# Kernel tuning notes

Hardware: AMD Instinct MI355X
Metric: run time of the kernel (lower is better)

## Reference

```python
import jax, jax.numpy as jnp
import numpy as np

MD = 4            # max_displacement
DP = 1            # dilation_patch
PATCH = 2 * MD + 1  # 9
# kernel_size=1, stride=1, padding=0, dilation=1 -> oH=H, oW=W


def setup_inputs() -> dict:
    key = jax.random.key(0)
    k1, k2 = jax.random.split(key)
    N, C, H, W = 8, 256, 128, 128
    input1 = jax.random.normal(k1, (N, C, H, W), dtype=jnp.float32)
    input2 = jax.random.normal(k2, (N, C, H, W), dtype=jnp.float32)
    return {"input1": input1, "input2": input2}


def _correlation(input1, input2):
    # out[n, py, px, y, x] = sum_c input1[n,c,y,x] * input2[n,c, y+(py-MD)*DP, x+(px-MD)*DP]
    # with zero padding for out-of-bounds input2 positions (mmcv semantics, no
    # normalization by channel count).
    N, C, H, W = input1.shape
    pad = MD * DP
    x2 = jnp.pad(input2, ((0, 0), (0, 0), (pad, pad), (pad, pad)))
    rows = []
    for py in range(PATCH):  # small fixed displacement grid (9x9)
        cols = []
        for px in range(PATCH):
            sh, sw = py * DP, px * DP
            x2s = x2[:, :, sh:sh + H, sw:sw + W]  # shifted input2, [N,C,H,W]
            cols.append(jnp.einsum('nchw,nchw->nhw', input1, x2s))
        rows.append(jnp.stack(cols, axis=1))  # [N, PATCH, H, W]
    return jnp.stack(rows, axis=1)  # [N, PATCH, PATCH, H, W]


def reference(input1, input2):
    return _correlation(input1, input2)
```

## Files before the change

### kernel.cpp

```cpp
#include <hip/hip_runtime.h>
#include <limits.h>

typedef __attribute__((ext_vector_type(8))) short short8v;
typedef __attribute__((ext_vector_type(4))) float f32x4;

#define H_  128
#define W_  128
#define C_  256
#define HW_ 16384

#define MFMA32(a, b, c) __builtin_amdgcn_mfma_f32_16x16x32_bf16(a, b, c, 0, 0, 0)

__device__ __forceinline__ short bf16b(float f) {
    unsigned u = __float_as_uint(f);
    u += 0x7fffu + ((u >> 16) & 1u);
    return (short)(u >> 16);
}
__device__ __forceinline__ unsigned bf16pk(float lo, float hi) {
    unsigned ul = __float_as_uint(lo);
    ul += 0x7fffu + ((ul >> 16) & 1u);
    unsigned uh = __float_as_uint(hi);
    uh += 0x7fffu + ((uh >> 16) & 1u);
    return (ul >> 16) | (uh & 0xffff0000u);
}

__global__ __launch_bounds__(512, 2)
void corr_kernel(const float* __restrict__ in1, const float* __restrict__ in2,
                 float* __restrict__ out)
{
    __shared__ __attribute__((aligned(16))) unsigned char smem[3 * 49152];
    short*    lds  = (short*)smem;
    unsigned* ldsI = (unsigned*)smem;
    float*    ldso = (float*)smem;

    const int tid  = threadIdx.x;
    const int lane = tid & 63;
    const int wid  = tid >> 6;
    const int m    = lane & 15;
    const int g    = lane >> 4;

    int bid = blockIdx.x;
    int swz = (bid & 7) * 64 + (bid >> 3);
    int n   = swz >> 6;
    int h0  = ((swz >> 3) & 7) << 4;
    int w0  = (swz & 7) << 4;

    const float* in1n = in1 + (size_t)n * (C_ * HW_);
    const float* in2n = in2 + (size_t)n * (C_ * HW_);

    int lwdw[5]; int gof0[5];
#pragma unroll
    for (int s = 0; s < 5; ++s) {
        int u    = tid + s * 512;
        bool act = (u < 2304);
        int q    = u % 6;
        int rest = u / 6;
        int kp   = rest & 15;
        int r    = rest >> 4;
        int row  = h0 - 4 + r;
        int col0 = w0 - 4 + 4 * q;
        bool inb = act && ((unsigned)row < 128u) && ((unsigned)col0 < 125u);
        int  cc  = 8 * (kp >> 2) + 2 * (kp & 3);
        gof0[s]  = inb ? (cc * HW_ + row * W_ + col0) : INT_MIN;
        lwdw[s]  = ((r * 4 + (kp >> 2)) * 32 + 4 * q) * 4 + (kp & 3);
    }
    const int abase = (8 * g) * HW_ + (h0 + 2 * wid) * W_ + (w0 + m);

    {
        short8v z = (short8v)0;
        short8v* zp = (short8v*)lds;
#pragma unroll
        for (int i = 0; i < 18; ++i) zp[tid + i * 512] = z;
    }

    f32x4 acc[2][9][2];
#pragma unroll
    for (int a = 0; a < 2; ++a)
#pragma unroll
        for (int d = 0; d < 9; ++d)
#pragma unroll
            for (int t = 0; t < 2; ++t)
                acc[a][d][t] = (f32x4){0.f, 0.f, 0.f, 0.f};

    __syncthreads();
    __builtin_amdgcn_sched_barrier(0);

    f32x4 sf[5][2];
    float afn[2][8];

#pragma unroll
    for (int s = 0; s < 5; ++s)
#pragma unroll
        for (int e = 0; e < 2; ++e) {
            f32x4 v = (f32x4){0.f, 0.f, 0.f, 0.f};
            if (gof0[s] != INT_MIN) v = *(const f32x4*)(in2n + gof0[s] + e * HW_);
            sf[s][e] = v;
        }
#pragma unroll
    for (int s = 0; s < 5; ++s)
        if (tid + s * 512 < 2304) {
#pragma unroll
            for (int d = 0; d < 4; ++d)
                ldsI[lwdw[s] + 4 * d] = bf16pk(sf[s][0][d], sf[s][1][d]);
        }
#pragma unroll
    for (int s = 0; s < 5; ++s)
#pragma unroll
        for (int e = 0; e < 2; ++e) {
            f32x4 v = (f32x4){0.f, 0.f, 0.f, 0.f};
            if (gof0[s] != INT_MIN) v = *(const f32x4*)(in2n + gof0[s] + e * HW_ + 32 * HW_);
            sf[s][e] = v;
        }
#pragma unroll
    for (int rs = 0; rs < 2; ++rs)
#pragma unroll
        for (int i = 0; i < 8; ++i)
            afn[rs][i] = in1n[abase + i * HW_ + rs * W_];

#pragma unroll 1
    for (int t = 0; t < 8; ++t) {
        __syncthreads();
        __builtin_amdgcn_sched_barrier(0);
        const int bcur  = t % 3;
        const int wnext = (t + 1) % 3;

        short8v a8[2];
#pragma unroll
        for (int rs = 0; rs < 2; ++rs)
#pragma unroll
            for (int i = 0; i < 8; ++i) a8[rs][i] = bf16b(afn[rs][i]);

        if (t < 7) {
            unsigned* wp = ldsI + wnext * 12288;
#pragma unroll
            for (int s = 0; s < 5; ++s)
                if (tid + s * 512 < 2304) {
#pragma unroll
                    for (int d = 0; d < 4; ++d)
                        wp[lwdw[s] + 4 * d] = bf16pk(sf[s][0][d], sf[s][1][d]);
                }
        }
        if (t < 6) {
            const int koff = (t + 2) * 32 * HW_;
#pragma unroll
            for (int s = 0; s < 5; ++s)
#pragma unroll
                for (int e = 0; e < 2; ++e) {
                    f32x4 v = (f32x4){0.f, 0.f, 0.f, 0.f};
                    if (gof0[s] != INT_MIN) v = *(const f32x4*)(in2n + gof0[s] + e * HW_ + koff);
                    sf[s][e] = v;
                }
        }
        if (t < 7) {
            const int akoff = (t + 1) * 32 * HW_;
#pragma unroll
            for (int rs = 0; rs < 2; ++rs)
#pragma unroll
                for (int i = 0; i < 8; ++i)
                    afn[rs][i] = in1n[abase + (akoff + i * HW_) + rs * W_];
        }

        const short* lb = lds + bcur * 24576;
#pragma unroll
        for (int rr = 0; rr < 10; ++rr) {
            int ro = (((2 * wid + rr) * 4 + g) * 32) * 8;
            short8v b0 = *(const short8v*)&lb[ro + m * 8];
            short8v b1 = *(const short8v*)&lb[ro + (16 + m) * 8];
            if (rr <= 8) {
                acc[0][rr][0] = MFMA32(a8[0], b0, acc[0][rr][0]);
                acc[0][rr][1] = MFMA32(a8[0], b1, acc[0][rr][1]);
            }
            if (rr >= 1) {
                acc[1][rr - 1][0] = MFMA32(a8[1], b0, acc[1][rr - 1][0]);
                acc[1][rr - 1][1] = MFMA32(a8[1], b1, acc[1][rr - 1][1]);
            }
        }
    }

    const size_t outb = (size_t)n * 81 * HW_;
#pragma unroll
    for (int dy = 0; dy < 9; ++dy) {
        __syncthreads();
        __builtin_amdgcn_sched_barrier(0);
#pragma unroll
        for (int rs = 0; rs < 2; ++rs) {
            int hl = 2 * wid + rs;
#pragma unroll
            for (int nt = 0; nt < 2; ++nt) {
#pragma unroll
                for (int i = 0; i < 4; ++i) {
                    int mm = 4 * g + i;
                    int dx = nt * 16 + m - mm;
                    if (dx >= 0 && dx < 9)
                        ldso[dx * 257 + hl * 16 + mm] = acc[rs][dy][nt][i];
                }
            }
        }
        __syncthreads();
        __builtin_amdgcn_sched_barrier(0);
#pragma unroll
        for (int e = 0; e < 5; ++e) {
            int t = tid + e * 512;
            if (t < 2304) {
                int dx  = t >> 8;
                int rem = t & 255;
                out[outb + (size_t)(dy * 9 + dx) * HW_ +
                    (size_t)(h0 + (rem >> 4)) * W_ + (w0 + (rem & 15))] = ldso[dx * 257 + rem];
            }
        }
    }
}

extern "C" void kernel_launch(void* const* d_in, const int* in_sizes, int n_in,
                              void* d_out, int out_size, void* d_ws, size_t ws_size,
                              hipStream_t stream) {
    const float* in1 = (const float*)d_in[0];
    const float* in2 = (const float*)d_in[1];
    float* out = (float*)d_out;
    corr_kernel<<<dim3(512), dim3(512), 0, stream>>>(in1, in2, out);
}
```

Measured before the change: 98.24 us.

## Use 1024-thread blocks with single LDS buffer, swizzled layout, and one-shot epilogue

Doubles the threads per block to 1024 so each wave owns a single output row instead of two, halving per-thread accumulators and register pressure. The triple-buffered LDS staging is replaced by a single buffer with two barriers per K step, using a rotated (XOR-like) dword layout to avoid bank conflicts instead of zero-initialised padding. The epilogue stages all 81 displacement planes in LDS at once and writes them out in a single pass instead of nine barrier-separated passes. This trades software pipelining depth for more waves and fewer per-thread registers, and may expose global load latency more.

```diff
diff --git a/kernel.cpp b/kernel.cpp
--- a/kernel.cpp
+++ b/kernel.cpp
@@ -4,9 +4,7 @@
 typedef __attribute__((ext_vector_type(8))) short short8v;
 typedef __attribute__((ext_vector_type(4))) float f32x4;
 
-#define H_  128
 #define W_  128
-#define C_  256
 #define HW_ 16384
 
 #define MFMA32(a, b, c) __builtin_amdgcn_mfma_f32_16x16x32_bf16(a, b, c, 0, 0, 0)
@@ -24,11 +22,11 @@
     return (ul >> 16) | (uh & 0xffff0000u);
 }
 
-__global__ __launch_bounds__(512, 2)
+__global__ __launch_bounds__(1024)
 void corr_kernel(const float* __restrict__ in1, const float* __restrict__ in2,
                  float* __restrict__ out)
 {
-    __shared__ __attribute__((aligned(16))) unsigned char smem[3 * 49152];
+    __shared__ __attribute__((aligned(16))) unsigned char smem[84992];
     short*    lds  = (short*)smem;
     unsigned* ldsI = (unsigned*)smem;
     float*    ldso = (float*)smem;
@@ -45,51 +43,41 @@
     int h0  = ((swz >> 3) & 7) << 4;
     int w0  = (swz & 7) << 4;
 
-    const float* in1n = in1 + (size_t)n * (C_ * HW_);
-    const float* in2n = in2 + (size_t)n * (C_ * HW_);
+    const float* in1n = in1 + (size_t)n * (256 * HW_);
+    const float* in2n = in2 + (size_t)n * (256 * HW_);
 
-    int lwdw[5]; int gof0[5];
+    int gof0[3], wbas[3], wrot[3];
+    bool act[3];
 #pragma unroll
-    for (int s = 0; s < 5; ++s) {
-        int u    = tid + s * 512;
-        bool act = (u < 2304);
+    for (int s = 0; s < 3; ++s) {
+        int u    = tid + s * 1024;
+        act[s]   = (u < 2304);
         int q    = u % 6;
         int rest = u / 6;
         int kp   = rest & 15;
         int r    = rest >> 4;
         int row  = h0 - 4 + r;
         int col0 = w0 - 4 + 4 * q;
-        bool inb = act && ((unsigned)row < 128u) && ((unsigned)col0 < 125u);
+        bool inb = act[s] && ((unsigned)row < 128u) && ((unsigned)col0 < 125u);
         int  cc  = 8 * (kp >> 2) + 2 * (kp & 3);
         gof0[s]  = inb ? (cc * HW_ + row * W_ + col0) : INT_MIN;
-        lwdw[s]  = ((r * 4 + (kp >> 2)) * 32 + 4 * q) * 4 + (kp & 3);
+        int rj   = r * 4 + (kp >> 2);
+        wbas[s]  = rj * 128;
+        wrot[s]  = 16 * q + (kp & 3) + ((rj & 7) << 2);
     }
-    const int abase = (8 * g) * HW_ + (h0 + 2 * wid) * W_ + (w0 + m);
+    const int abase = (8 * g) * HW_ + (h0 + wid) * W_ + (w0 + m);
 
-    {
-        short8v z = (short8v)0;
-        short8v* zp = (short8v*)lds;
+    f32x4 acc[9][2];
 #pragma unroll
-        for (int i = 0; i < 18; ++i) zp[tid + i * 512] = z;
-    }
+    for (int d = 0; d < 9; ++d)
+#pragma unroll
+        for (int t = 0; t < 2; ++t)
+            acc[d][t] = (f32x4){0.f, 0.f, 0.f, 0.f};
 
-    f32x4 acc[2][9][2];
+    f32x4 sf[3][2];
+    float af[8];
 #pragma unroll
-    for (int a = 0; a < 2; ++a)
-#pragma unroll
-        for (int d = 0; d < 9; ++d)
-#pragma unroll
-            for (int t = 0; t < 2; ++t)
-                acc[a][d][t] = (f32x4){0.f, 0.f, 0.f, 0.f};
-
-    __syncthreads();
-    __builtin_amdgcn_sched_barrier(0);
-
-    f32x4 sf[5][2];
-    float afn[2][8];
-
-#pragma unroll
-    for (int s = 0; s < 5; ++s)
+    for (int s = 0; s < 3; ++s)
 #pragma unroll
         for (int e = 0; e < 2; ++e) {
             f32x4 v = (f32x4){0.f, 0.f, 0.f, 0.f};
@@ -97,53 +85,47 @@
             sf[s][e] = v;
         }
 #pragma unroll
-    for (int s = 0; s < 5; ++s)
-        if (tid + s * 512 < 2304) {
-#pragma unroll
-            for (int d = 0; d < 4; ++d)
-                ldsI[lwdw[s] + 4 * d] = bf16pk(sf[s][0][d], sf[s][1][d]);
-        }
-#pragma unroll
-    for (int s = 0; s < 5; ++s)
-#pragma unroll
-        for (int e = 0; e < 2; ++e) {
-            f32x4 v = (f32x4){0.f, 0.f, 0.f, 0.f};
-            if (gof0[s] != INT_MIN) v = *(const f32x4*)(in2n + gof0[s] + e * HW_ + 32 * HW_);
-            sf[s][e] = v;
-        }
-#pragma unroll
-    for (int rs = 0; rs < 2; ++rs)
-#pragma unroll
-        for (int i = 0; i < 8; ++i)
-            afn[rs][i] = in1n[abase + i * HW_ + rs * W_];
+    for (int i = 0; i < 8; ++i) af[i] = in1n[abase + i * HW_];
 
 #pragma unroll 1
     for (int t = 0; t < 8; ++t) {
+#pragma unroll
+        for (int s = 0; s < 3; ++s)
+            if (act[s]) {
+#pragma unroll
+                for (int d = 0; d < 4; ++d)
+                    ldsI[wbas[s] + ((wrot[s] + 4 * d) & 127)] =
+                        bf16pk(sf[s][0][d], sf[s][1][d]);
+            }
         __syncthreads();
         __builtin_amdgcn_sched_barrier(0);
-        const int bcur  = t % 3;
-        const int wnext = (t + 1) % 3;
 
-        short8v a8[2];
+        short8v a8;
 #pragma unroll
-        for (int rs = 0; rs < 2; ++rs)
+        for (int i = 0; i < 8; ++i) a8[i] = bf16b(af[i]);
+        if (t < 7) {
+            const int koff = (t + 1) * 32 * HW_;
 #pragma unroll
-            for (int i = 0; i < 8; ++i) a8[rs][i] = bf16b(afn[rs][i]);
+            for (int i = 0; i < 8; ++i) af[i] = in1n[abase + koff + i * HW_];
+        }
+
+#pragma unroll
+        for (int dy = 0; dy < 9; ++dy) {
+            int rj   = (wid + dy) * 4 + g;
+            int base = rj * 128;
+            int rot  = (rj & 7) << 2;
+#pragma unroll
+            for (int nt = 0; nt < 2; ++nt) {
+                int dw = base + ((((nt * 16 + m) << 2) + rot) & 127);
+                short8v b = *(const short8v*)&lds[dw * 2];
+                acc[dy][nt] = MFMA32(a8, b, acc[dy][nt]);
+            }
+        }
 
         if (t < 7) {
-            unsigned* wp = ldsI + wnext * 12288;
+            const int koff = (t + 1) * 32 * HW_;
 #pragma unroll
-            for (int s = 0; s < 5; ++s)
-                if (tid + s * 512 < 2304) {
-#pragma unroll
-                    for (int d = 0; d < 4; ++d)
-                        wp[lwdw[s] + 4 * d] = bf16pk(sf[s][0][d], sf[s][1][d]);
-                }
-        }
-        if (t < 6) {
-            const int koff = (t + 2) * 32 * HW_;
-#pragma unroll
-            for (int s = 0; s < 5; ++s)
+            for (int s = 0; s < 3; ++s)
 #pragma unroll
                 for (int e = 0; e < 2; ++e) {
                     f32x4 v = (f32x4){0.f, 0.f, 0.f, 0.f};
@@ -151,62 +133,34 @@
                     sf[s][e] = v;
                 }
         }
-        if (t < 7) {
-            const int akoff = (t + 1) * 32 * HW_;
+        __syncthreads();
+        __builtin_amdgcn_sched_barrier(0);
+    }
+
 #pragma unroll
-            for (int rs = 0; rs < 2; ++rs)
+    for (int dy = 0; dy < 9; ++dy) {
 #pragma unroll
-                for (int i = 0; i < 8; ++i)
-                    afn[rs][i] = in1n[abase + (akoff + i * HW_) + rs * W_];
-        }
-
-        const short* lb = lds + bcur * 24576;
+        for (int nt = 0; nt < 2; ++nt) {
 #pragma unroll
-        for (int rr = 0; rr < 10; ++rr) {
-            int ro = (((2 * wid + rr) * 4 + g) * 32) * 8;
-            short8v b0 = *(const short8v*)&lb[ro + m * 8];
-            short8v b1 = *(const short8v*)&lb[ro + (16 + m) * 8];
-            if (rr <= 8) {
-                acc[0][rr][0] = MFMA32(a8[0], b0, acc[0][rr][0]);
-                acc[0][rr][1] = MFMA32(a8[0], b1, acc[0][rr][1]);
-            }
-            if (rr >= 1) {
-                acc[1][rr - 1][0] = MFMA32(a8[1], b0, acc[1][rr - 1][0]);
-                acc[1][rr - 1][1] = MFMA32(a8[1], b1, acc[1][rr - 1][1]);
+            for (int i = 0; i < 4; ++i) {
+                int mm = 4 * g + i;
+                int dx = nt * 16 + m - mm;
+                if (dx >= 0 && dx < 9)
+                    ldso[(dy * 9 + dx) * 260 + wid * 16 + mm] = acc[dy][nt][i];
             }
         }
     }
-
+    __syncthreads();
+    __builtin_amdgcn_sched_barrier(0);
     const size_t outb = (size_t)n * 81 * HW_;
 #pragma unroll
-    for (int dy = 0; dy < 9; ++dy) {
-        __syncthreads();
-        __builtin_amdgcn_sched_barrier(0);
-#pragma unroll
-        for (int rs = 0; rs < 2; ++rs) {
-            int hl = 2 * wid + rs;
-#pragma unroll
-            for (int nt = 0; nt < 2; ++nt) {
-#pragma unroll
-                for (int i = 0; i < 4; ++i) {
-                    int mm = 4 * g + i;
-                    int dx = nt * 16 + m - mm;
-                    if (dx >= 0 && dx < 9)
-                        ldso[dx * 257 + hl * 16 + mm] = acc[rs][dy][nt][i];
-                }
-            }
-        }
-        __syncthreads();
-        __builtin_amdgcn_sched_barrier(0);
-#pragma unroll
-        for (int e = 0; e < 5; ++e) {
-            int t = tid + e * 512;
-            if (t < 2304) {
-                int dx  = t >> 8;
-                int rem = t & 255;
-                out[outb + (size_t)(dy * 9 + dx) * HW_ +
-                    (size_t)(h0 + (rem >> 4)) * W_ + (w0 + (rem & 15))] = ldso[dx * 257 + rem];
-            }
+    for (int e = 0; e < 21; ++e) {
+        int t2 = tid + e * 1024;
+        if (t2 < 20736) {
+            int dydx = t2 >> 8;
+            int rem  = t2 & 255;
+            out[outb + (size_t)dydx * HW_ +
+                (size_t)(h0 + (rem >> 4)) * W_ + (w0 + (rem & 15))] = ldso[dydx * 260 + rem];
         }
     }
 }
@@ -217,5 +171,5 @@
     const float* in1 = (const float*)d_in[0];
     const float* in2 = (const float*)d_in[1];
     float* out = (float*)d_out;
-    corr_kernel<<<dim3(512), dim3(512), 0, stream>>>(in1, in2, out);
+    corr_kernel<<<dim3(512), dim3(1024), 0, stream>>>(in1, in2, out);
 }
```

After: 176.6 us. 1.8x slower.

## Restructure LDS staging with swizzled vector writes, double buffering, and a batched epilogue

Applied to the files above, without the earlier changes.

Replaces the triple-buffered scalar LDS fill with double buffering. Each thread now loads 8 channels and writes packed 16-byte bf16 vectors into a rotation-swizzled layout, which is meant to cut LDS store count and bank conflicts. Global loads for the next K chunk are issued before the MFMA loop and converted afterwards, so load latency overlaps compute. The epilogue stages all 81 displacement planes in LDS at once, replacing 18 barriers with one before writing out. The trade-off is higher register pressure from the larger prefetch arrays, and the code leaves a few leftover no-op statements.

```diff
diff --git a/kernel.cpp b/kernel.cpp
--- a/kernel.cpp
+++ b/kernel.cpp
@@ -3,19 +3,13 @@
 
 typedef __attribute__((ext_vector_type(8))) short short8v;
 typedef __attribute__((ext_vector_type(4))) float f32x4;
-
-#define H_  128
+typedef __attribute__((ext_vector_type(4))) unsigned u32x4;
+
 #define W_  128
-#define C_  256
 #define HW_ 16384
 
 #define MFMA32(a, b, c) __builtin_amdgcn_mfma_f32_16x16x32_bf16(a, b, c, 0, 0, 0)
 
-__device__ __forceinline__ short bf16b(float f) {
-    unsigned u = __float_as_uint(f);
-    u += 0x7fffu + ((u >> 16) & 1u);
-    return (short)(u >> 16);
-}
 __device__ __forceinline__ unsigned bf16pk(float lo, float hi) {
     unsigned ul = __float_as_uint(lo);
     ul += 0x7fffu + ((ul >> 16) & 1u);
@@ -28,10 +22,9 @@
 void corr_kernel(const float* __restrict__ in1, const float* __restrict__ in2,
                  float* __restrict__ out)
 {
-    __shared__ __attribute__((aligned(16))) unsigned char smem[3 * 49152];
-    short*    lds  = (short*)smem;
-    unsigned* ldsI = (unsigned*)smem;
-    float*    ldso = (float*)smem;
+    __shared__ __attribute__((aligned(16))) unsigned char smem[98304];
+    short* lds  = (short*)smem;
+    float* ldso = (float*)smem;
 
     const int tid  = threadIdx.x;
     const int lane = tid & 63;
@@ -45,33 +38,27 @@
     int h0  = ((swz >> 3) & 7) << 4;
     int w0  = (swz & 7) << 4;
 
-    const float* in1n = in1 + (size_t)n * (C_ * HW_);
-    const float* in2n = in2 + (size_t)n * (C_ * HW_);
-
-    int lwdw[5]; int gof0[5];
-#pragma unroll
-    for (int s = 0; s < 5; ++s) {
+    const float* in1n = in1 + (size_t)n * (256 * HW_);
+    const float* in2n = in2 + (size_t)n * (256 * HW_);
+
+    int gofs[2], wrow[2], wcp0[2];
+    bool act[2];
+#pragma unroll
+    for (int s = 0; s < 2; ++s) {
         int u    = tid + s * 512;
-        bool act = (u < 2304);
-        int q    = u % 6;
-        int rest = u / 6;
-        int kp   = rest & 15;
-        int r    = rest >> 4;
+        act[s]   = (u < 576);
+        int cg   = u % 6;
+        int rj   = u / 6;
+        int r    = rj >> 2;
+        int j    = rj & 3;
         int row  = h0 - 4 + r;
-        int col0 = w0 - 4 + 4 * q;
-        bool inb = act && ((unsigned)row < 128u) && ((unsigned)col0 < 125u);
-        int  cc  = 8 * (kp >> 2) + 2 * (kp & 3);
-        gof0[s]  = inb ? (cc * HW_ + row * W_ + col0) : INT_MIN;
-        lwdw[s]  = ((r * 4 + (kp >> 2)) * 32 + 4 * q) * 4 + (kp & 3);
+        int col0 = w0 - 4 + 4 * cg;
+        bool inb = act[s] && ((unsigned)row < 128u) && ((unsigned)col0 < 125u);
+        gofs[s]  = inb ? ((8 * j) * HW_ + row * W_ + col0) : INT_MIN;
+        wrow[s]  = rj * 256;
+        wcp0[s]  = 4 * cg + rj;
     }
     const int abase = (8 * g) * HW_ + (h0 + 2 * wid) * W_ + (w0 + m);
-
-    {
-        short8v z = (short8v)0;
-        short8v* zp = (short8v*)lds;
-#pragma unroll
-        for (int i = 0; i < 18; ++i) zp[tid + i * 512] = z;
-    }
 
     f32x4 acc[2][9][2];
 #pragma unroll
@@ -82,109 +69,131 @@
             for (int t = 0; t < 2; ++t)
                 acc[a][d][t] = (f32x4){0.f, 0.f, 0.f, 0.f};
 
+    {
+        f32x4 v[2][8];
+        float af0[2][8];
+#pragma unroll
+        for (int s = 0; s < 2; ++s)
+#pragma unroll
+            for (int i = 0; i < 8; ++i) {
+                f32x4 x = (f32x4){0.f, 0.f, 0.f, 0.f};
+                if (gofs[s] != INT_MIN) x = *(const f32x4*)(in2n + gofs[s] + i * HW_);
+                v[s][i] = x;
+            }
+#pragma unroll
+        for (int rs = 0; rs < 2; ++rs)
+#pragma unroll
+            for (int i = 0; i < 8; ++i)
+                af0[rs][i] = in1n[abase + rs * W_ + i * HW_];
+#pragma unroll
+        for (int s = 0; s < 2; ++s)
+            if (act[s]) {
+#pragma unroll
+                for (int d = 0; d < 4; ++d) {
+                    u32x4 pk;
+#pragma unroll
+                    for (int h = 0; h < 4; ++h)
+                        pk[h] = bf16pk(v[s][2 * h][d], v[s][2 * h + 1][d]);
+                    *(u32x4*)&lds[wrow[s] + ((wcp0[s] + d) & 31) * 8] = pk;
+                }
+            }
+        (void)0;
+#pragma unroll
+        for (int rs = 0; rs < 2; ++rs)
+#pragma unroll
+            for (int i = 0; i < 8; ++i)
+                ;
+        extern __shared__ unsigned char _dummy[]; (void)_dummy;
+        __syncthreads();
+        u32x4 anP[2];
+#pragma unroll
+        for (int rs = 0; rs < 2; ++rs) {
+            u32x4 pk;
+#pragma unroll
+            for (int h = 0; h < 4; ++h)
+                pk[h] = bf16pk(af0[rs][2 * h], af0[rs][2 * h + 1]);
+            anP[rs] = pk;
+        }
+
+#pragma unroll 1
+        for (int t = 0; t < 8; ++t) {
+            f32x4 vn[2][8];
+            float afn[2][8];
+            if (t < 7) {
+                const int koff = (t + 1) * 32 * HW_;
+#pragma unroll
+                for (int s = 0; s < 2; ++s)
+#pragma unroll
+                    for (int i = 0; i < 8; ++i) {
+                        f32x4 x = (f32x4){0.f, 0.f, 0.f, 0.f};
+                        if (gofs[s] != INT_MIN)
+                            x = *(const f32x4*)(in2n + gofs[s] + koff + i * HW_);
+                        vn[s][i] = x;
+                    }
+#pragma unroll
+                for (int rs = 0; rs < 2; ++rs)
+#pragma unroll
+                    for (int i = 0; i < 8; ++i)
+                        afn[rs][i] = in1n[abase + koff + rs * W_ + i * HW_];
+            }
+
+            if (t > 0) __syncthreads();
+
+            short8v a8[2];
+#pragma unroll
+            for (int rs = 0; rs < 2; ++rs) {
+                u32x4 tmp = anP[rs];
+                a8[rs] = *reinterpret_cast<short8v*>(&tmp);
+            }
+
+            const short* lb = lds + (t & 1) * 24576;
+#pragma unroll
+            for (int rr = 0; rr < 10; ++rr) {
+                int rj2 = (2 * wid + rr) * 4 + g;
+                int ro  = rj2 * 256;
+                short8v b0 = *(const short8v*)&lb[ro + ((m + rj2) & 31) * 8];
+                short8v b1 = *(const short8v*)&lb[ro + ((16 + m + rj2) & 31) * 8];
+                if (rr <= 8) {
+                    acc[0][rr][0] = MFMA32(a8[0], b0, acc[0][rr][0]);
+                    acc[0][rr][1] = MFMA32(a8[0], b1, acc[0][rr][1]);
+                }
+                if (rr >= 1) {
+                    acc[1][rr - 1][0] = MFMA32(a8[1], b0, acc[1][rr - 1][0]);
+                    acc[1][rr - 1][1] = MFMA32(a8[1], b1, acc[1][rr - 1][1]);
+                }
+            }
+
+            if (t < 7) {
+                short* wb = lds + ((t + 1) & 1) * 24576;
+#pragma unroll
+                for (int s = 0; s < 2; ++s)
+                    if (act[s]) {
+#pragma unroll
+                        for (int d = 0; d < 4; ++d) {
+                            u32x4 pk;
+#pragma unroll
+                            for (int h = 0; h < 4; ++h)
+                                pk[h] = bf16pk(vn[s][2 * h][d], vn[s][2 * h + 1][d]);
+                            *(u32x4*)&wb[wrow[s] + ((wcp0[s] + d) & 31) * 8] = pk;
+                        }
+                    }
+#pragma unroll
+                for (int rs = 0; rs < 2; ++rs) {
+                    u32x4 pk;
+#pragma unroll
+                    for (int h = 0; h < 4; ++h)
+                        pk[h] = bf16pk(afn[rs][2 * h], afn[rs][2 * h + 1]);
+                    anP[rs] = pk;
+                }
+            }
+        }
+    }
+
     __syncthreads();
-    __builtin_amdgcn_sched_barrier(0);
-
-    f32x4 sf[5][2];
-    float afn[2][8];
-
-#pragma unroll
-    for (int s = 0; s < 5; ++s)
-#pragma unroll
-        for (int e = 0; e < 2; ++e) {
-            f32x4 v = (f32x4){0.f, 0.f, 0.f, 0.f};
-            if (gof0[s] != INT_MIN) v = *(const f32x4*)(in2n + gof0[s] + e * HW_);
-            sf[s][e] = v;
-        }
-#pragma unroll
-    for (int s = 0; s < 5; ++s)
-        if (tid + s * 512 < 2304) {
-#pragma unroll
-            for (int d = 0; d < 4; ++d)
-                ldsI[lwdw[s] + 4 * d] = bf16pk(sf[s][0][d], sf[s][1][d]);
-        }
-#pragma unroll
-    for (int s = 0; s < 5; ++s)
-#pragma unroll
-        for (int e = 0; e < 2; ++e) {
-            f32x4 v = (f32x4){0.f, 0.f, 0.f, 0.f};
-            if (gof0[s] != INT_MIN) v = *(const f32x4*)(in2n + gof0[s] + e * HW_ + 32 * HW_);
-            sf[s][e] = v;
-        }
-#pragma unroll
-    for (int rs = 0; rs < 2; ++rs)
-#pragma unroll
-        for (int i = 0; i < 8; ++i)
-            afn[rs][i] = in1n[abase + i * HW_ + rs * W_];
-
-#pragma unroll 1
-    for (int t = 0; t < 8; ++t) {
-        __syncthreads();
-        __builtin_amdgcn_sched_barrier(0);
-        const int bcur  = t % 3;
-        const int wnext = (t + 1) % 3;
-
-        short8v a8[2];
-#pragma unroll
-        for (int rs = 0; rs < 2; ++rs)
-#pragma unroll
-            for (int i = 0; i < 8; ++i) a8[rs][i] = bf16b(afn[rs][i]);
-
-        if (t < 7) {
-            unsigned* wp = ldsI + wnext * 12288;
-#pragma unroll
-            for (int s = 0; s < 5; ++s)
-                if (tid + s * 512 < 2304) {
-#pragma unroll
-                    for (int d = 0; d < 4; ++d)
-                        wp[lwdw[s] + 4 * d] = bf16pk(sf[s][0][d], sf[s][1][d]);
-                }
-        }
-        if (t < 6) {
-            const int koff = (t + 2) * 32 * HW_;
-#pragma unroll
-            for (int s = 0; s < 5; ++s)
-#pragma unroll
-                for (int e = 0; e < 2; ++e) {
-                    f32x4 v = (f32x4){0.f, 0.f, 0.f, 0.f};
-                    if (gof0[s] != INT_MIN) v = *(const f32x4*)(in2n + gof0[s] + e * HW_ + koff);
-                    sf[s][e] = v;
-                }
-        }
-        if (t < 7) {
-            const int akoff = (t + 1) * 32 * HW_;
-#pragma unroll
-            for (int rs = 0; rs < 2; ++rs)
-#pragma unroll
-                for (int i = 0; i < 8; ++i)
-                    afn[rs][i] = in1n[abase + (akoff + i * HW_) + rs * W_];
-        }
-
-        const short* lb = lds + bcur * 24576;
-#pragma unroll
-        for (int rr = 0; rr < 10; ++rr) {
-            int ro = (((2 * wid + rr) * 4 + g) * 32) * 8;
-            short8v b0 = *(const short8v*)&lb[ro + m * 8];
-            short8v b1 = *(const short8v*)&lb[ro + (16 + m) * 8];
-            if (rr <= 8) {
-                acc[0][rr][0] = MFMA32(a8[0], b0, acc[0][rr][0]);
-                acc[0][rr][1] = MFMA32(a8[0], b1, acc[0][rr][1]);
-            }
-            if (rr >= 1) {
-                acc[1][rr - 1][0] = MFMA32(a8[1], b0, acc[1][rr - 1][0]);
-                acc[1][rr - 1][1] = MFMA32(a8[1], b1, acc[1][rr - 1][1]);
-            }
-        }
-    }
-
-    const size_t outb = (size_t)n * 81 * HW_;
 #pragma unroll
     for (int dy = 0; dy < 9; ++dy) {
-        __syncthreads();
-        __builtin_amdgcn_sched_barrier(0);
 #pragma unroll
         for (int rs = 0; rs < 2; ++rs) {
-            int hl = 2 * wid + rs;
 #pragma unroll
             for (int nt = 0; nt < 2; ++nt) {
 #pragma unroll
@@ -192,21 +201,21 @@
                     int mm = 4 * g + i;
                     int dx = nt * 16 + m - mm;
                     if (dx >= 0 && dx < 9)
-                        ldso[dx * 257 + hl * 16 + mm] = acc[rs][dy][nt][i];
-                }
-            }
-        }
-        __syncthreads();
-        __builtin_amdgcn_sched_barrier(0);
-#pragma unroll
-        for (int e = 0; e < 5; ++e) {
-            int t = tid + e * 512;
-            if (t < 2304) {
-                int dx  = t >> 8;
-                int rem = t & 255;
-                out[outb + (size_t)(dy * 9 + dx) * HW_ +
-                    (size_t)(h0 + (rem >> 4)) * W_ + (w0 + (rem & 15))] = ldso[dx * 257 + rem];
-            }
+                        ldso[(dy * 9 + dx) * 257 + (2 * wid + rs) * 16 + mm] = acc[rs][dy][nt][i];
+                }
+            }
+        }
+    }
+    __syncthreads();
+    const size_t outb = (size_t)n * 81 * HW_;
+#pragma unroll
+    for (int e = 0; e < 41; ++e) {
+        int t2 = tid + e * 512;
+        if (t2 < 20736) {
+            int dydx = t2 >> 8;
+            int rem  = t2 & 255;
+            out[outb + (size_t)dydx * HW_ +
+                (size_t)(h0 + (rem >> 4)) * W_ + (w0 + (rem & 15))] = ldso[dydx * 257 + rem];
         }
     }
 }
```

Result: slower. 160.9 us (+63.7%).
